# Kernel optimization log

Hardware: AMD Instinct MI355X
Metric: run time of the kernel (lower is better)

The kernel has to match this reference:

```python
import jax, jax.numpy as jnp
import numpy as np

# ---- static config (mirrors SynthesisLayer __init__ with chosen init_kwargs) ----
B, CIN, COUT, H, W, WDIM = 8, 512, 512, 64, 64, 512
K = 3                      # conv_kernel (not torgb)
UP, DOWN = 2, 2            # tmp_fs=128 vs in/out fs=64
TAPS = 12                  # filter_size * factor
PX0, PX1, PY0, PY1 = 9, 8, 9, 8   # from the padding formula in __init__
CLAMP = 256.0
SLOPE = 0.2
LRELU_GAIN = float(np.sqrt(2.0))
IN_CUTOFF, IN_HALFW = 16.0, 16.0
OUT_CUTOFF, OUT_HALFW = 16.0, 16.0
TMP_FS = 128.0


def _design_lowpass(numtaps, cutoff, width, fs):
    # numpy re-implementation of scipy.signal.firwin (Kaiser-window design)
    nyq = fs / 2.0
    m = np.arange(numtaps) - (numtaps - 1) / 2.0
    c = cutoff / nyq
    h = c * np.sinc(c * m)
    atten = 2.285 * (numtaps - 1) * np.pi * (width / nyq) + 7.95  # kaiser_atten
    if atten > 50:
        beta = 0.1102 * (atten - 8.7)
    elif atten > 21:
        beta = 0.5842 * (atten - 21) ** 0.4 + 0.07886 * (atten - 21)
    else:
        beta = 0.0
    h *= np.kaiser(numtaps, beta)
    h /= h.sum()
    return jnp.asarray(h, dtype=jnp.float32)


def _upfirdn2d_sep(x, f, up=1, down=1, padding=(0, 0, 0, 0), gain=1.0):
    # separable 1D filter applied along W then H; matches NVIDIA upfirdn2d ref
    C = x.shape[1]
    px0, px1, py0, py1 = padding
    f = f[::-1]  # flip_filter=False -> true convolution
    f = (f * np.sqrt(gain)).astype(x.dtype)  # gain ** (ndim/2) per 1D pass
    k = f.shape[0]
    dn = ('NCHW', 'OIHW', 'NCHW')
    # zero-upsample (trailing zeros) == lhs_dilation + (up-1) extra high pad
    kw = jnp.tile(f.reshape(1, 1, 1, k), (C, 1, 1, 1))
    x = jax.lax.conv_general_dilated(x, kw, (1, down), ((0, 0), (px0, px1 + up - 1)),
                                     lhs_dilation=(1, up), dimension_numbers=dn,
                                     feature_group_count=C)
    kh = jnp.tile(f.reshape(1, 1, k, 1), (C, 1, 1, 1))
    x = jax.lax.conv_general_dilated(x, kh, (down, 1), ((py0, py1 + up - 1), (0, 0)),
                                     lhs_dilation=(up, 1), dimension_numbers=dn,
                                     feature_group_count=C)
    return x


def _modulated_conv2d(x, w, s):
    # demodulate=True path; input_gain = rsqrt(magnitude_ema=1) = 1
    b, i, h, wid = x.shape
    o = w.shape[0]
    w = w * jax.lax.rsqrt(jnp.mean(jnp.square(w), axis=(1, 2, 3), keepdims=True))
    s = s * jax.lax.rsqrt(jnp.mean(jnp.square(s)))
    wb = w[None] * s[:, None, :, None, None]                      # [B,O,I,kh,kw]
    d = jax.lax.rsqrt(jnp.sum(jnp.square(wb), axis=(2, 3, 4)) + 1e-8)  # [B,O]
    wb = wb * d[:, :, None, None, None]
    xg = x.reshape(1, b * i, h, wid)
    wg = wb.reshape(b * o, i, K, K)
    y = jax.lax.conv_general_dilated(xg, wg, (1, 1), ((K - 1, K - 1), (K - 1, K - 1)),
                                     dimension_numbers=('NCHW', 'OIHW', 'NCHW'),
                                     feature_group_count=b)
    return y.reshape(b, o, h + K - 1, wid + K - 1)


def setup_inputs() -> dict:
    key = jax.random.key(0)
    ks = jax.random.split(key, 5)
    x = jax.random.normal(ks[0], (B, CIN, H, W), jnp.float32)
    w_lat = jax.random.normal(ks[1], (B, WDIM), jnp.float32)
    conv_w = jax.random.normal(ks[2], (COUT, CIN, K, K), jnp.float32)
    conv_b = jax.random.normal(ks[3], (COUT,), jnp.float32) * 0.1
    aff_w = jax.random.normal(ks[4], (CIN, WDIM), jnp.float32)
    aff_b = jnp.ones((CIN,), jnp.float32)  # style affine bias_init=1
    up_f = _design_lowpass(TAPS, IN_CUTOFF, 2 * IN_HALFW, TMP_FS)
    dn_f = _design_lowpass(TAPS, OUT_CUTOFF, 2 * OUT_HALFW, TMP_FS)
    return {"x": x, "w_lat": w_lat, "conv_w": conv_w, "conv_b": conv_b,
            "aff_w": aff_w, "aff_b": aff_b, "up_f": up_f, "dn_f": dn_f}


def reference(x, w_lat, conv_w, conv_b, aff_w, aff_b, up_f, dn_f):
    # affine (equalized linear, weight scale 1/sqrt(w_dim))
    styles = (w_lat @ aff_w.T) * (1.0 / np.sqrt(WDIM)) + aff_b
    y = _modulated_conv2d(x, conv_w, styles)                     # [B,O,66,66]
    # filtered_lrelu reference: bias -> clamp -> FIR up -> lrelu*gain -> clamp -> FIR down
    y = y + conv_b[None, :, None, None]
    y = jnp.clip(y, -CLAMP, CLAMP)
    y = _upfirdn2d_sep(y, up_f, up=UP, padding=(PX0, PX1, PY0, PY1), gain=UP * UP)
    y = jax.nn.leaky_relu(y, SLOPE) * LRELU_GAIN
    y = jnp.clip(y, -CLAMP, CLAMP)
    y = _upfirdn2d_sep(y, dn_f, down=DOWN)                       # [B,O,64,64]
    return y
```

## Files before the change

### kernel.cpp

```cpp
#include <hip/hip_runtime.h>
#include <stdint.h>

typedef short short8 __attribute__((ext_vector_type(8)));
typedef float f32x4 __attribute__((ext_vector_type(4)));

__device__ __forceinline__ unsigned short f2bf(float f) {
  union { float f; unsigned u; } v; v.f = f;
  unsigned u = v.u;
  u += 0x7fffu + ((u >> 16) & 1u);
  return (unsigned short)(u >> 16);
}

__device__ __forceinline__ void gl16(const void* g, void* l) {
  __builtin_amdgcn_global_load_lds(
      (__attribute__((address_space(1))) void*)(uintptr_t)g,
      (__attribute__((address_space(3))) void*)l, 16, 0, 0);
}

#define NSPAT 36992
#define PLANE 4624
#define XHP_ROWS 37152

__global__ void styles_kernel(const float* __restrict__ w_lat, const float* __restrict__ affw,
                              const float* __restrict__ affb, float* __restrict__ s) {
  int g = blockIdx.x * 256 + threadIdx.x;
  int b = g >> 9, i = g & 511;
  const float4* wl = (const float4*)(w_lat + b * 512);
  const float4* aw = (const float4*)(affw + (size_t)i * 512);
  float acc = 0.f;
#pragma unroll 4
  for (int j = 0; j < 128; ++j) {
    float4 a = wl[j], c = aw[j];
    acc += a.x * c.x + a.y * c.y + a.z * c.z + a.w * c.w;
  }
  s[g] = acc * 0.044194173824159216f + affb[i];
}

__global__ void norm_kernel(float* __restrict__ s, float* __restrict__ s2) {
  __shared__ float red[256];
  int t = threadIdx.x;
  float acc = 0.f;
  for (int e = t; e < 4096; e += 256) { float v = s[e]; acc += v * v; }
  red[t] = acc; __syncthreads();
  for (int st = 128; st > 0; st >>= 1) {
    if (t < st) red[t] += red[t + st];
    __syncthreads();
  }
  float alpha = rsqrtf(red[0] * (1.0f / 4096.0f));
  for (int e = t; e < 4096; e += 256) {
    float v = s[e] * alpha;
    s[e] = v; s2[e] = v * v;
  }
}

__global__ void rowscale_kernel(const float* __restrict__ convw, float* __restrict__ rowscale) {
  int o = blockIdx.x, t = threadIdx.x;
  const float* wr = convw + (size_t)o * 4608;
  float acc = 0.f;
  for (int e = t; e < 4608; e += 256) { float v = wr[e]; acc += v * v; }
  __shared__ float red[256];
  red[t] = acc; __syncthreads();
  for (int st = 128; st > 0; st >>= 1) {
    if (t < st) red[t] += red[t + st];
    __syncthreads();
  }
  if (t == 0) rowscale[o] = rsqrtf(red[0] * (1.0f / 4608.0f));
}

__global__ void wprep_kernel(const float* __restrict__ convw, const float* __restrict__ rowscale,
                             unsigned short* __restrict__ wbf, float* __restrict__ W2) {
  int o = blockIdx.x, t = threadIdx.x;
  float sc = rowscale[o];
  for (int i = t; i < 512; i += 256) {
    const float* wp = convw + ((size_t)o * 512 + i) * 9;
    float w9[9]; float ss = 0.f;
#pragma unroll
    for (int m = 0; m < 9; ++m) { float v = wp[m] * sc; w9[m] = v; ss += v * v; }
    W2[((size_t)o << 9) + i] = ss;
#pragma unroll
    for (int m = 0; m < 9; ++m)
      wbf[(((size_t)m * 512 + o) << 9) + i] = f2bf(w9[m]);
  }
}

__global__ void demod_kernel(const float* __restrict__ s2, const float* __restrict__ W2,
                             float* __restrict__ dbuf) {
  int g = blockIdx.x * 256 + threadIdx.x;
  int b = g >> 9, o = g & 511;
  const float4* sp = (const float4*)(s2 + b * 512);
  const float4* wp = (const float4*)(W2 + (size_t)o * 512);
  float acc = 1e-8f;
#pragma unroll 4
  for (int j = 0; j < 128; ++j) {
    float4 a = sp[j], c = wp[j];
    acc += a.x * c.x + a.y * c.y + a.z * c.z + a.w * c.w;
  }
  dbuf[g] = rsqrtf(acc);
}

__global__ void xprep_kernel(const float* __restrict__ x, const float* __restrict__ s,
                             unsigned short* __restrict__ xhp) {
  int b = blockIdx.x >> 6, h = blockIdx.x & 63;
  int t = threadIdx.x;
  __shared__ float tile[64 * 65];
  __shared__ float sv[64];
  for (int it = 0; it < 8; ++it) {
    int i0 = it * 64;
    {
      int ii = t >> 2, wseg = (t & 3) * 16;
      const float4* src = (const float4*)(x + (((size_t)(b * 512 + i0 + ii) * 64 + h) << 6) + wseg);
      float4 v0 = src[0], v1 = src[1], v2 = src[2], v3 = src[3];
      float* dst = tile + ii * 65 + wseg;
      dst[0]=v0.x; dst[1]=v0.y; dst[2]=v0.z; dst[3]=v0.w;
      dst[4]=v1.x; dst[5]=v1.y; dst[6]=v1.z; dst[7]=v1.w;
      dst[8]=v2.x; dst[9]=v2.y; dst[10]=v2.z; dst[11]=v2.w;
      dst[12]=v3.x; dst[13]=v3.y; dst[14]=v3.z; dst[15]=v3.w;
    }
    if (t < 64) sv[t] = s[b * 512 + i0 + t];
    __syncthreads();
    {
      int w = t >> 2, ic = (t & 3) * 16;
      alignas(16) unsigned short tmp[16];
#pragma unroll
      for (int k = 0; k < 16; ++k)
        tmp[k] = f2bf(tile[(ic + k) * 65 + w] * sv[ic + k]);
      unsigned short* dst = xhp + ((size_t)b * PLANE + (h + 2) * 68 + (w + 2)) * 512 + i0 + ic;
      *(short8*)dst = *(const short8*)tmp;
      *(short8*)(dst + 8) = *(const short8*)(tmp + 8);
    }
    __syncthreads();
  }
}

__global__ __launch_bounds__(256, 2) void conv_kernel(const unsigned short* __restrict__ wbf,
                                                      const unsigned short* __restrict__ xhp,
                                                      const float* __restrict__ dbuf,
                                                      const float* __restrict__ convb,
                                                      float* __restrict__ ybuf) {
  extern __shared__ unsigned short lds[];
  const int t = threadIdx.x;
  const int lane = t & 63, wid = t >> 6;

  int orig = blockIdx.y * 4 + blockIdx.x;
  int xcd = orig & 7, idx = orig >> 3;
  int wg = (xcd < 4) ? (xcd * 145 + idx) : (580 + (xcd - 4) * 144 + idx);
  const int n0 = (wg >> 2) * 128, o0 = (wg & 3) * 128;
  const int wm = wid >> 1, wn = wid & 1;

  const unsigned kcq = (((unsigned)(lane & 3)) ^ ((unsigned)(lane >> 3) & 3u)) * 8u;
  const unsigned aSrc = (unsigned)(o0 + wid * 16 + (lane >> 2)) * 512 + kcq;
  const unsigned bSrc = (unsigned)(n0 + wid * 16 + (lane >> 2)) * 512 + kcq;

  const unsigned xq = ((unsigned)(lane >> 4)) ^ (((unsigned)(lane & 15) >> 1) & 3u);
  const unsigned aRd = (unsigned)(wm * 64 + (lane & 15)) * 32 + xq * 8;
  const unsigned bRd = (unsigned)(wn * 64 + (lane & 15)) * 32 + xq * 8;

  f32x4 acc[4][4] = {};

#define STAGE(kt, bufb) do {                                            \
    const unsigned kti = (unsigned)(kt);                                \
    const unsigned tap = kti >> 3, k0e = (kti & 7u) * 64u;              \
    const unsigned aB = tap * 262144u + k0e;                            \
    const unsigned bB = ((tap / 3u) * 68u + (tap % 3u)) * 512u + k0e;   \
    unsigned short* lb = lds + (bufb) * 16384 + wid * 512;              \
    gl16(wbf + aB + aSrc,              lb);                             \
    gl16(wbf + aB + aSrc + 32768,      lb + 2048);                      \
    gl16(wbf + aB + 32 + aSrc,         lb + 4096);                      \
    gl16(wbf + aB + 32 + aSrc + 32768, lb + 6144);                      \
    gl16(xhp + bB + bSrc,              lb + 8192);                      \
    gl16(xhp + bB + bSrc + 32768,      lb + 10240);                     \
    gl16(xhp + bB + 32 + bSrc,         lb + 12288);                     \
    gl16(xhp + bB + 32 + bSrc + 32768, lb + 14336);                     \
  } while (0)

#define COMPUTE_KK(bufb, kk) do {                                       \
    const unsigned short* aF = lds + (bufb) * 16384 + (kk) * 4096 + aRd;        \
    const unsigned short* bF = lds + (bufb) * 16384 + 8192 + (kk) * 4096 + bRd; \
    short8 a0 = *(const short8*)(aF + 0);                               \
    short8 a1 = *(const short8*)(aF + 512);                             \
    short8 a2 = *(const short8*)(aF + 1024);                            \
    short8 a3 = *(const short8*)(aF + 1536);                            \
    short8 b0 = *(const short8*)(bF + 0);                               \
    short8 b1 = *(const short8*)(bF + 512);                             \
    short8 b2 = *(const short8*)(bF + 1024);                            \
    short8 b3 = *(const short8*)(bF + 1536);                            \
    __builtin_amdgcn_s_setprio(1);                                      \
    acc[0][0] = __builtin_amdgcn_mfma_f32_16x16x32_bf16(a0, b0, acc[0][0], 0, 0, 0); \
    acc[0][1] = __builtin_amdgcn_mfma_f32_16x16x32_bf16(a0, b1, acc[0][1], 0, 0, 0); \
    acc[0][2] = __builtin_amdgcn_mfma_f32_16x16x32_bf16(a0, b2, acc[0][2], 0, 0, 0); \
    acc[0][3] = __builtin_amdgcn_mfma_f32_16x16x32_bf16(a0, b3, acc[0][3], 0, 0, 0); \
    acc[1][0] = __builtin_amdgcn_mfma_f32_16x16x32_bf16(a1, b0, acc[1][0], 0, 0, 0); \
    acc[1][1] = __builtin_amdgcn_mfma_f32_16x16x32_bf16(a1, b1, acc[1][1], 0, 0, 0); \
    acc[1][2] = __builtin_amdgcn_mfma_f32_16x16x32_bf16(a1, b2, acc[1][2], 0, 0, 0); \
    acc[1][3] = __builtin_amdgcn_mfma_f32_16x16x32_bf16(a1, b3, acc[1][3], 0, 0, 0); \
    acc[2][0] = __builtin_amdgcn_mfma_f32_16x16x32_bf16(a2, b0, acc[2][0], 0, 0, 0); \
    acc[2][1] = __builtin_amdgcn_mfma_f32_16x16x32_bf16(a2, b1, acc[2][1], 0, 0, 0); \
    acc[2][2] = __builtin_amdgcn_mfma_f32_16x16x32_bf16(a2, b2, acc[2][2], 0, 0, 0); \
    acc[2][3] = __builtin_amdgcn_mfma_f32_16x16x32_bf16(a2, b3, acc[2][3], 0, 0, 0); \
    acc[3][0] = __builtin_amdgcn_mfma_f32_16x16x32_bf16(a3, b0, acc[3][0], 0, 0, 0); \
    acc[3][1] = __builtin_amdgcn_mfma_f32_16x16x32_bf16(a3, b1, acc[3][1], 0, 0, 0); \
    acc[3][2] = __builtin_amdgcn_mfma_f32_16x16x32_bf16(a3, b2, acc[3][2], 0, 0, 0); \
    acc[3][3] = __builtin_amdgcn_mfma_f32_16x16x32_bf16(a3, b3, acc[3][3], 0, 0, 0); \
    __builtin_amdgcn_s_setprio(0);                                      \
  } while (0)

  STAGE(0, 0);

  for (int k = 0; k < 72; ++k) {
    asm volatile("s_waitcnt vmcnt(0)" ::: "memory");
    __builtin_amdgcn_s_barrier();
    asm volatile("" ::: "memory");
    if (k < 71) STAGE(k + 1, (k + 1) & 1);
    __builtin_amdgcn_sched_barrier(0);
    COMPUTE_KK(k & 1, 0);
    COMPUTE_KK(k & 1, 1);
    asm volatile("" ::: "memory");
  }
#undef STAGE
#undef COMPUTE_KK

  const int col = lane & 15;
  const int rbase = (lane >> 4) * 4;
#pragma unroll
  for (int ni = 0; ni < 4; ++ni) {
    const unsigned n = (unsigned)(n0 + wn * 64 + ni * 16 + col);
    const unsigned b = n / 4624u;
    const float* dr = dbuf + b * 512;
#pragma unroll
    for (int mi = 0; mi < 4; ++mi) {
      const int ob = o0 + wm * 64 + mi * 16 + rbase;
#pragma unroll
      for (int j = 0; j < 4; ++j) {
        const int o = ob + j;
        float v = acc[mi][ni][j] * dr[o] + convb[o];
        v = fminf(fmaxf(v, -256.f), 256.f);
        ybuf[(size_t)o * NSPAT + n] = v;
      }
    }
  }
}

__global__ __launch_bounds__(256, 4) void updown_kernel(const float* __restrict__ ybuf,
                                                        const float* __restrict__ upf,
                                                        const float* __restrict__ dnf,
                                                        float* __restrict__ out) {
  __shared__ float sm[9880];
  float* uhB = sm;
  float* uB  = sm + 5016;
  float* dvT = sm + 5016;

  const int blk = blockIdx.x;
  const int half = blk & 1, ch = blk >> 1;
  const int o = ch & 511, b = ch >> 9;
  const float* ybase = ybuf + (size_t)o * NSPAT + b * PLANE;
  const int t = threadIdx.x;
  const int uc0 = half * 32 - 4;

  float f2[12], g[12];
#pragma unroll
  for (int m = 0; m < 12; ++m) { f2[m] = upf[11 - m] * 2.0f; g[m] = dnf[11 - m]; }

  for (int u = t; u < 726; u += 256) {
    int p = u / 11, q = u - p * 11;
    int gc = uc0 + 4 * q;
    f32x4 v = {0.f, 0.f, 0.f, 0.f};
    if (gc >= 0 && gc < 66) {
      v = *(const f32x4*)(ybase + p * 68 + gc);
#pragma unroll
      for (int j = 0; j < 4; ++j)
        if (gc + j >= 66) v[j] = 0.f;
    }
    *(f32x4*)(uB + p * 44 + 4 * q) = v;
  }
  __syncthreads();

  for (int u = t; u < 1254; u += 256) {
    int p = u / 19, cq = u - p * 19;
    const float* ur = uB + p * 44 + 2 * cq;
    float R0 = ur[0], R1 = ur[1], R2 = ur[2], R3 = ur[3], R4 = ur[4], R5 = ur[5], R6 = ur[6];
    f32x4 o4;
    o4[0] = f2[1]*R0 + f2[3]*R1 + f2[5]*R2 + f2[7]*R3 + f2[9]*R4 + f2[11]*R5;
    o4[1] = f2[0]*R0 + f2[2]*R1 + f2[4]*R2 + f2[6]*R3 + f2[8]*R4 + f2[10]*R5;
    o4[2] = f2[1]*R1 + f2[3]*R2 + f2[5]*R3 + f2[7]*R4 + f2[9]*R5 + f2[11]*R6;
    o4[3] = f2[0]*R1 + f2[2]*R2 + f2[4]*R3 + f2[6]*R4 + f2[8]*R5 + f2[10]*R6;
    *(f32x4*)(uhB + p * 76 + 4 * cq) = o4;
  }
  __syncthreads();

  if (t < 225) {
    const int cl = t % 75, sg = t / 75;
    const int s0 = sg * 22;
    const int ttg0 = 2 * s0;
    float R[32];
#pragma unroll
    for (int k = 0; k < 32; ++k) {
      int j = s0 - 4 + k;
      R[k] = (j >= 0 && j < 66) ? uhB[j * 76 + cl] : 0.f;
    }
    float dv[22];
#pragma unroll
    for (int m = 0; m < 22; ++m) dv[m] = 0.f;
#pragma unroll
    for (int k = 0; k < 54; ++k) {
      const int kb = k >> 1;
      float z;
      if (k & 1)
        z = f2[0]*R[kb] + f2[2]*R[kb+1] + f2[4]*R[kb+2] + f2[6]*R[kb+3] + f2[8]*R[kb+4] + f2[10]*R[kb+5];
      else
        z = f2[1]*R[kb] + f2[3]*R[kb+1] + f2[5]*R[kb+2] + f2[7]*R[kb+3] + f2[9]*R[kb+4] + f2[11]*R[kb+5];
      z = (z > 0.f ? z : 0.2f * z) * 1.4142135623730951f;
      z = fminf(fmaxf(z, -256.f), 256.f);
      if (ttg0 + k >= 138) z = 0.f;
      const int mlo = (k < 11) ? 0 : ((k - 10) >> 1);
      const int mhi = ((k >> 1) < 21) ? (k >> 1) : 21;
#pragma unroll
      for (int m = mlo; m <= mhi; ++m)
        dv[m] += g[k - 2 * m] * z;
    }
#pragma unroll
    for (int m = 0; m < 22; ++m) {
      const int s = s0 + m;
      if (s < 64) dvT[s * 76 + cl] = dv[m];
    }
  }
  __syncthreads();

  {
    const int s = t >> 2, rq = t & 3;
    const float* dr = dvT + s * 76 + 16 * rq;
    f32x4 dd[7];
#pragma unroll
    for (int i = 0; i < 7; ++i) dd[i] = *(const f32x4*)(dr + 4 * i);
    float D[28];
#pragma unroll
    for (int i = 0; i < 7; ++i) {
      D[4*i+0] = dd[i][0]; D[4*i+1] = dd[i][1]; D[4*i+2] = dd[i][2]; D[4*i+3] = dd[i][3];
    }
    f32x4 o0, o1;
#pragma unroll
    for (int m = 0; m < 8; ++m) {
      float v = g[0]*D[2*m] + g[1]*D[2*m+1] + g[2]*D[2*m+2] + g[3]*D[2*m+3]
              + g[4]*D[2*m+4] + g[5]*D[2*m+5] + g[6]*D[2*m+6] + g[7]*D[2*m+7]
              + g[8]*D[2*m+8] + g[9]*D[2*m+9] + g[10]*D[2*m+10] + g[11]*D[2*m+11];
      if (m < 4) o0[m] = v; else o1[m - 4] = v;
    }
    float* ob = out + (((size_t)(b * 512 + o)) << 12) + s * 64 + half * 32 + 8 * rq;
    *(f32x4*)ob = o0;
    *(f32x4*)(ob + 4) = o1;
  }
}

extern "C" void kernel_launch(void* const* d_in, const int* in_sizes, int n_in,
                              void* d_out, int out_size, void* d_ws, size_t ws_size,
                              hipStream_t stream) {
  const float* x     = (const float*)d_in[0];
  const float* w_lat = (const float*)d_in[1];
  const float* convw = (const float*)d_in[2];
  const float* convb = (const float*)d_in[3];
  const float* affw  = (const float*)d_in[4];
  const float* affb  = (const float*)d_in[5];
  const float* upf   = (const float*)d_in[6];
  const float* dnf   = (const float*)d_in[7];
  float* out = (float*)d_out;

  char* ws = (char*)d_ws;
  float* s         = (float*)(ws + 0);
  float* s2        = (float*)(ws + 16384);
  float* rowscale  = (float*)(ws + 32768);
  float* W2        = (float*)(ws + 34816);
  float* dbuf      = (float*)(ws + 1083392);
  unsigned short* wbf = (unsigned short*)(ws + 1099776);
  unsigned short* xhp = (unsigned short*)(ws + 5818368);
  float* ybuf      = (float*)(ws + 43862016);

  styles_kernel<<<16, 256, 0, stream>>>(w_lat, affw, affb, s);
  norm_kernel<<<1, 256, 0, stream>>>(s, s2);
  rowscale_kernel<<<512, 256, 0, stream>>>(convw, rowscale);
  wprep_kernel<<<512, 256, 0, stream>>>(convw, rowscale, wbf, W2);
  demod_kernel<<<16, 256, 0, stream>>>(s2, W2, dbuf);

  hipMemsetAsync(xhp, 0, (size_t)XHP_ROWS * 512 * 2, stream);
  xprep_kernel<<<512, 256, 0, stream>>>(x, s, xhp);

  dim3 cgrid(4, 289);
  conv_kernel<<<cgrid, 256, 65536, stream>>>(wbf, xhp, dbuf, convb, ybuf);

  updown_kernel<<<8192, 256, 0, stream>>>(ybuf, upf, dnf, out);
}
```

Measured before the change: 362.1 us.

## Store conv output in fp16, retile updown, remap conv grid, fuse weight prep

The conv epilogue now writes the intermediate activation as fp16 instead of fp32. This halves the traffic between the conv kernel and the up/down filter kernel. The updown kernel is split into quarter-width blocks with smaller shared memory and higher occupancy. The conv grid becomes 1D with an XCD-aware tile mapping, padded to 1168 blocks with a bounds guard and an enlarged xhp buffer. The rowscale and wprep kernels are merged into one launch. The fp16 intermediate adds rounding error on values clamped to ±256, and the narrower updown tiles recompute more halo.

```diff
diff --git a/kernel.cpp b/kernel.cpp
--- a/kernel.cpp
+++ b/kernel.cpp
@@ -1,4 +1,5 @@
 #include <hip/hip_runtime.h>
+#include <hip/hip_fp16.h>
 #include <stdint.h>
 
 typedef short short8 __attribute__((ext_vector_type(8)));
@@ -19,7 +20,7 @@
 
 #define NSPAT 36992
 #define PLANE 4624
-#define XHP_ROWS 37152
+#define XHP_ROWS 37520
 
 __global__ void styles_kernel(const float* __restrict__ w_lat, const float* __restrict__ affw,
                               const float* __restrict__ affb, float* __restrict__ s) {
@@ -53,7 +54,8 @@
   }
 }
 
-__global__ void rowscale_kernel(const float* __restrict__ convw, float* __restrict__ rowscale) {
+__global__ void wprep_kernel(const float* __restrict__ convw,
+                             unsigned short* __restrict__ wbf, float* __restrict__ W2) {
   int o = blockIdx.x, t = threadIdx.x;
   const float* wr = convw + (size_t)o * 4608;
   float acc = 0.f;
@@ -64,13 +66,7 @@
     if (t < st) red[t] += red[t + st];
     __syncthreads();
   }
-  if (t == 0) rowscale[o] = rsqrtf(red[0] * (1.0f / 4608.0f));
-}
-
-__global__ void wprep_kernel(const float* __restrict__ convw, const float* __restrict__ rowscale,
-                             unsigned short* __restrict__ wbf, float* __restrict__ W2) {
-  int o = blockIdx.x, t = threadIdx.x;
-  float sc = rowscale[o];
+  float sc = rsqrtf(red[0] * (1.0f / 4608.0f));
   for (int i = t; i < 512; i += 256) {
     const float* wp = convw + ((size_t)o * 512 + i) * 9;
     float w9[9]; float ss = 0.f;
@@ -136,15 +132,17 @@
                                                       const unsigned short* __restrict__ xhp,
                                                       const float* __restrict__ dbuf,
                                                       const float* __restrict__ convb,
-                                                      float* __restrict__ ybuf) {
+                                                      __half* __restrict__ ybuf) {
   extern __shared__ unsigned short lds[];
   const int t = threadIdx.x;
   const int lane = t & 63, wid = t >> 6;
 
-  int orig = blockIdx.y * 4 + blockIdx.x;
-  int xcd = orig & 7, idx = orig >> 3;
-  int wg = (xcd < 4) ? (xcd * 145 + idx) : (580 + (xcd - 4) * 144 + idx);
-  const int n0 = (wg >> 2) * 128, o0 = (wg & 3) * 128;
+  const int orig = blockIdx.x;
+  const int xcd = orig & 7, idx = orig >> 3;
+  const int q = xcd & 3, s = xcd >> 2;
+  const int nt = q * 73 + (idx >> 1);
+  const int ot = 2 * s + (idx & 1);
+  const int n0 = nt * 128, o0 = ot * 128;
   const int wm = wid >> 1, wn = wid & 1;
 
   const unsigned kcq = (((unsigned)(lane & 3)) ^ ((unsigned)(lane >> 3) & 3u)) * 8u;
@@ -219,89 +217,95 @@
 #undef STAGE
 #undef COMPUTE_KK
 
-  const int col = lane & 15;
-  const int rbase = (lane >> 4) * 4;
-#pragma unroll
-  for (int ni = 0; ni < 4; ++ni) {
-    const unsigned n = (unsigned)(n0 + wn * 64 + ni * 16 + col);
-    const unsigned b = n / 4624u;
-    const float* dr = dbuf + b * 512;
-#pragma unroll
-    for (int mi = 0; mi < 4; ++mi) {
-      const int ob = o0 + wm * 64 + mi * 16 + rbase;
-#pragma unroll
-      for (int j = 0; j < 4; ++j) {
-        const int o = ob + j;
-        float v = acc[mi][ni][j] * dr[o] + convb[o];
-        v = fminf(fmaxf(v, -256.f), 256.f);
-        ybuf[(size_t)o * NSPAT + n] = v;
+  if (n0 < NSPAT) {
+    const int col = lane & 15;
+    const int rbase = (lane >> 4) * 4;
+#pragma unroll
+    for (int ni = 0; ni < 4; ++ni) {
+      const unsigned n = (unsigned)(n0 + wn * 64 + ni * 16 + col);
+      const unsigned b = n / 4624u;
+      const float* dr = dbuf + b * 512;
+#pragma unroll
+      for (int mi = 0; mi < 4; ++mi) {
+        const int ob = o0 + wm * 64 + mi * 16 + rbase;
+#pragma unroll
+        for (int j = 0; j < 4; ++j) {
+          const int o = ob + j;
+          float v = acc[mi][ni][j] * dr[o] + convb[o];
+          v = fminf(fmaxf(v, -256.f), 256.f);
+          ybuf[(size_t)o * NSPAT + n] = __float2half(v);
+        }
       }
     }
   }
 }
 
-__global__ __launch_bounds__(256, 4) void updown_kernel(const float* __restrict__ ybuf,
+__global__ __launch_bounds__(256, 6) void updown_kernel(const __half* __restrict__ ybuf,
                                                         const float* __restrict__ upf,
                                                         const float* __restrict__ dnf,
                                                         float* __restrict__ out) {
-  __shared__ float sm[9880];
+  __shared__ float sm[5720];
   float* uhB = sm;
-  float* uB  = sm + 5016;
-  float* dvT = sm + 5016;
+  float* uB  = sm + 2904;
+  float* dvT = sm + 2904;
 
   const int blk = blockIdx.x;
-  const int half = blk & 1, ch = blk >> 1;
+  const int h = blk & 3, ch = blk >> 2;
   const int o = ch & 511, b = ch >> 9;
-  const float* ybase = ybuf + (size_t)o * NSPAT + b * PLANE;
+  const __half* ybase = ybuf + (size_t)o * NSPAT + b * PLANE;
   const int t = threadIdx.x;
-  const int uc0 = half * 32 - 4;
+  const int gc0 = 16 * h - 4;
 
   float f2[12], g[12];
 #pragma unroll
   for (int m = 0; m < 12; ++m) { f2[m] = upf[11 - m] * 2.0f; g[m] = dnf[11 - m]; }
 
-  for (int u = t; u < 726; u += 256) {
-    int p = u / 11, q = u - p * 11;
-    int gc = uc0 + 4 * q;
+  for (int u = t; u < 462; u += 256) {
+    int p = u / 7, qd = u - p * 7;
+    int gc = gc0 + 4 * qd;
     f32x4 v = {0.f, 0.f, 0.f, 0.f};
     if (gc >= 0 && gc < 66) {
-      v = *(const f32x4*)(ybase + p * 68 + gc);
+      const __half* src = ybase + p * 68 + gc;
+      __half2 h0 = *(const __half2*)(src);
+      __half2 h1 = *(const __half2*)(src + 2);
+      float2 f0 = __half22float2(h0), f1 = __half22float2(h1);
+      v[0] = f0.x; v[1] = f0.y; v[2] = f1.x; v[3] = f1.y;
 #pragma unroll
       for (int j = 0; j < 4; ++j)
         if (gc + j >= 66) v[j] = 0.f;
     }
-    *(f32x4*)(uB + p * 44 + 4 * q) = v;
+    *(f32x4*)(uB + p * 28 + 4 * qd) = v;
   }
   __syncthreads();
 
-  for (int u = t; u < 1254; u += 256) {
-    int p = u / 19, cq = u - p * 19;
-    const float* ur = uB + p * 44 + 2 * cq;
+  for (int u = t; u < 726; u += 256) {
+    int p = u / 11, cq = u - p * 11;
+    const float* ur = uB + p * 28 + 2 * cq;
     float R0 = ur[0], R1 = ur[1], R2 = ur[2], R3 = ur[3], R4 = ur[4], R5 = ur[5], R6 = ur[6];
     f32x4 o4;
     o4[0] = f2[1]*R0 + f2[3]*R1 + f2[5]*R2 + f2[7]*R3 + f2[9]*R4 + f2[11]*R5;
     o4[1] = f2[0]*R0 + f2[2]*R1 + f2[4]*R2 + f2[6]*R3 + f2[8]*R4 + f2[10]*R5;
     o4[2] = f2[1]*R1 + f2[3]*R2 + f2[5]*R3 + f2[7]*R4 + f2[9]*R5 + f2[11]*R6;
     o4[3] = f2[0]*R1 + f2[2]*R2 + f2[4]*R3 + f2[6]*R4 + f2[8]*R5 + f2[10]*R6;
-    *(f32x4*)(uhB + p * 76 + 4 * cq) = o4;
+    *(f32x4*)(uhB + p * 44 + 4 * cq) = o4;
   }
   __syncthreads();
 
-  if (t < 225) {
-    const int cl = t % 75, sg = t / 75;
-    const int s0 = sg * 22;
+  if (t < 252) {
+    const int cl = t % 42, sg = t / 42;
+    const int s0 = sg * 11;
     const int ttg0 = 2 * s0;
-    float R[32];
+    float R[21];
+#pragma unroll
+    for (int i = 0; i < 21; ++i) {
+      int j = s0 - 4 + i;
+      R[i] = (j >= 0 && j < 66) ? uhB[j * 44 + cl] : 0.f;
+    }
+    float dv[11];
+#pragma unroll
+    for (int m = 0; m < 11; ++m) dv[m] = 0.f;
 #pragma unroll
     for (int k = 0; k < 32; ++k) {
-      int j = s0 - 4 + k;
-      R[k] = (j >= 0 && j < 66) ? uhB[j * 76 + cl] : 0.f;
-    }
-    float dv[22];
-#pragma unroll
-    for (int m = 0; m < 22; ++m) dv[m] = 0.f;
-#pragma unroll
-    for (int k = 0; k < 54; ++k) {
       const int kb = k >> 1;
       float z;
       if (k & 1)
@@ -311,42 +315,38 @@
       z = (z > 0.f ? z : 0.2f * z) * 1.4142135623730951f;
       z = fminf(fmaxf(z, -256.f), 256.f);
       if (ttg0 + k >= 138) z = 0.f;
-      const int mlo = (k < 11) ? 0 : ((k - 10) >> 1);
-      const int mhi = ((k >> 1) < 21) ? (k >> 1) : 21;
+      const int mlo = (k < 12) ? 0 : ((k - 10) >> 1);
+      const int mhi = (kb < 10) ? kb : 10;
 #pragma unroll
       for (int m = mlo; m <= mhi; ++m)
         dv[m] += g[k - 2 * m] * z;
     }
 #pragma unroll
-    for (int m = 0; m < 22; ++m) {
+    for (int m = 0; m < 11; ++m) {
       const int s = s0 + m;
-      if (s < 64) dvT[s * 76 + cl] = dv[m];
+      if (s < 64) dvT[s * 44 + cl] = dv[m];
     }
   }
   __syncthreads();
 
   {
     const int s = t >> 2, rq = t & 3;
-    const float* dr = dvT + s * 76 + 16 * rq;
-    f32x4 dd[7];
-#pragma unroll
-    for (int i = 0; i < 7; ++i) dd[i] = *(const f32x4*)(dr + 4 * i);
-    float D[28];
-#pragma unroll
-    for (int i = 0; i < 7; ++i) {
-      D[4*i+0] = dd[i][0]; D[4*i+1] = dd[i][1]; D[4*i+2] = dd[i][2]; D[4*i+3] = dd[i][3];
-    }
-    f32x4 o0, o1;
-#pragma unroll
-    for (int m = 0; m < 8; ++m) {
+    const float* dr = dvT + s * 44 + 8 * rq;
+    float D[20];
+#pragma unroll
+    for (int i = 0; i < 5; ++i) {
+      f32x4 dd = *(const f32x4*)(dr + 4 * i);
+      D[4*i+0] = dd[0]; D[4*i+1] = dd[1]; D[4*i+2] = dd[2]; D[4*i+3] = dd[3];
+    }
+    f32x4 o4;
+#pragma unroll
+    for (int m = 0; m < 4; ++m) {
       float v = g[0]*D[2*m] + g[1]*D[2*m+1] + g[2]*D[2*m+2] + g[3]*D[2*m+3]
               + g[4]*D[2*m+4] + g[5]*D[2*m+5] + g[6]*D[2*m+6] + g[7]*D[2*m+7]
               + g[8]*D[2*m+8] + g[9]*D[2*m+9] + g[10]*D[2*m+10] + g[11]*D[2*m+11];
-      if (m < 4) o0[m] = v; else o1[m - 4] = v;
-    }
-    float* ob = out + (((size_t)(b * 512 + o)) << 12) + s * 64 + half * 32 + 8 * rq;
-    *(f32x4*)ob = o0;
-    *(f32x4*)(ob + 4) = o1;
+      o4[m] = v;
+    }
+    *(f32x4*)(out + (((size_t)(b * 512 + o)) << 12) + s * 64 + 16 * h + 4 * rq) = o4;
   }
 }
 
@@ -366,24 +366,21 @@
   char* ws = (char*)d_ws;
   float* s         = (float*)(ws + 0);
   float* s2        = (float*)(ws + 16384);
-  float* rowscale  = (float*)(ws + 32768);
   float* W2        = (float*)(ws + 34816);
   float* dbuf      = (float*)(ws + 1083392);
   unsigned short* wbf = (unsigned short*)(ws + 1099776);
   unsigned short* xhp = (unsigned short*)(ws + 5818368);
-  float* ybuf      = (float*)(ws + 43862016);
+  __half* ybuf     = (__half*)(ws + 44238848);
 
   styles_kernel<<<16, 256, 0, stream>>>(w_lat, affw, affb, s);
   norm_kernel<<<1, 256, 0, stream>>>(s, s2);
-  rowscale_kernel<<<512, 256, 0, stream>>>(convw, rowscale);
-  wprep_kernel<<<512, 256, 0, stream>>>(convw, rowscale, wbf, W2);
+  wprep_kernel<<<512, 256, 0, stream>>>(convw, wbf, W2);
   demod_kernel<<<16, 256, 0, stream>>>(s2, W2, dbuf);
 
   hipMemsetAsync(xhp, 0, (size_t)XHP_ROWS * 512 * 2, stream);
   xprep_kernel<<<512, 256, 0, stream>>>(x, s, xhp);
 
-  dim3 cgrid(4, 289);
-  conv_kernel<<<cgrid, 256, 65536, stream>>>(wbf, xhp, dbuf, convb, ybuf);
-
-  updown_kernel<<<8192, 256, 0, stream>>>(ybuf, upf, dnf, out);
-}
+  conv_kernel<<<1168, 256, 65536, stream>>>(wbf, xhp, dbuf, convb, ybuf);
+
+  updown_kernel<<<16384, 256, 0, stream>>>(ybuf, upf, dnf, out);
+}
```

New measurement: 372.3 us. 1.03x slower.
